# Kernel tuning notes

Measured on AMD Instinct MI355X. Metric: run time of the kernel, lower is better.

## Reference

```python
import jax, jax.numpy as jnp
import numpy as np

B, IN, H = 64, 1024, 1024

def setup_inputs() -> dict:
    key = jax.random.key(0)
    ks = jax.random.split(key, 16)
    s = 0.02
    inp = {
        'x': jax.random.normal(ks[0], (B, IN), dtype=jnp.float32),
        'C': jax.random.normal(ks[1], (B, H, H), dtype=jnp.float32) * 0.1,
        'n': jax.random.normal(ks[2], (B, H), dtype=jnp.float32) * 0.1,
        'm': jnp.zeros((B, H), dtype=jnp.float32),
    }
    names = ['i', 'f', 'o', 'q', 'k', 'v']
    for j, nm in enumerate(names):
        inp['W_' + nm] = jax.random.normal(ks[3 + 2 * j], (H, IN), dtype=jnp.float32) * s
        inp['b_' + nm] = jax.random.normal(ks[4 + 2 * j], (H,), dtype=jnp.float32) * s
    return inp

def reference(x, C, n, m, W_i, b_i, W_f, b_f, W_o, b_o, W_q, b_q, W_k, b_k, W_v, b_v):
    lin = lambda W, b: x @ W.T + b  # (B, H)
    i_tilda = lin(W_i, b_i)
    f_tilda = lin(W_f, b_f)
    o_tilda = lin(W_o, b_o)
    q_t = lin(W_q, b_q)
    k_t = lin(W_k, b_k) / jnp.sqrt(jnp.asarray(H, dtype=x.dtype))
    v_t = lin(W_v, b_v)

    f_t = jax.nn.sigmoid(f_tilda)
    o_t = jax.nn.sigmoid(o_tilda)
    # m_t = max(log(f_t) + m, log(exp(i_tilda))) = max(log_sigmoid(f_tilda) + m, i_tilda)
    m_t = jnp.maximum(jnp.log(f_t) + m, i_tilda)
    i_prime = jnp.exp(i_tilda - m_t)

    # Outer-product fast-weight update: C_t[b,i,k] = f*C + i' * v[b,i] k[b,k]
    C_t = f_t[:, :, None] * C + i_prime[:, :, None] * jnp.einsum('bi,bk->bik', v_t, k_t)
    n_t = f_t * n + i_prime * k_t

    # diagonal(n_t @ q_t.T) == per-row dot product
    normalize_inner = jnp.sum(n_t * q_t, axis=-1)
    divisor = jnp.maximum(jnp.abs(normalize_inner), jnp.ones_like(normalize_inner))
    h_tilda = jnp.einsum('bkj,bj->bk', C_t, q_t) / divisor[:, None]
    h_t = o_t * h_tilda
    return (h_t, C_t, n_t, m_t)
```

## Files before the change

### kernel.cpp

```cpp
#include <hip/hip_runtime.h>
#include <math.h>

#define BB 64
#define HH 1024
#define KK 1024

#define OFF_H ((size_t)0)
#define OFF_C ((size_t)BB * HH)
#define OFF_N (OFF_C + (size_t)BB * HH * HH)
#define OFF_M (OFF_N + (size_t)BB * HH)

#define SPLITK 4
#define GBN 32
#define GBK 64
#define NCOLBLK (6 * HH / GBN)

typedef float __attribute__((ext_vector_type(4))) f32x4;

__device__ __forceinline__ float dot4v(f32x4 a, f32x4 b) {
    return a[0] * b[0] + a[1] * b[1] + a[2] * b[2] + a[3] * b[3];
}
__device__ __forceinline__ void fma4(float4& a, const float4 x, const float4 w) {
    a.x = fmaf(x.x, w.x, a.x);
    a.y = fmaf(x.y, w.y, a.y);
    a.z = fmaf(x.z, w.z, a.z);
    a.w = fmaf(x.w, w.w, a.w);
}
__device__ __forceinline__ f32x4 ntload4(const float* p) {
    return __builtin_nontemporal_load((const f32x4*)p);
}
__device__ __forceinline__ f32x4 ld4(const float* p) {
    return *(const f32x4*)p;
}
__device__ __forceinline__ void ntstore4(float* p, f32x4 v) {
    __builtin_nontemporal_store(v, (f32x4*)p);
}

__global__ __launch_bounds__(256) void k_gemm(
    const float* __restrict__ x,
    const float* __restrict__ Wi, const float* __restrict__ Wf,
    const float* __restrict__ Wo, const float* __restrict__ Wq,
    const float* __restrict__ Wk, const float* __restrict__ Wv,
    float* __restrict__ Gp)
{
    const int cb = blockIdx.x % NCOLBLK;
    const int kc = blockIdx.x / NCOLBLK;
    const int n0 = cb * GBN;
    const int g  = n0 >> 10;
    const int h0 = n0 & (HH - 1);
    const int k0 = kc * (KK / SPLITK);

    const float* W = (g == 0) ? Wi : (g == 1) ? Wf : (g == 2) ? Wo
                   : (g == 3) ? Wq : (g == 4) ? Wk : Wv;

    const int tid = threadIdx.x;
    const int tn  = tid & 15;
    const int tm  = tid >> 4;

    __shared__ float sW[GBN][GBK + 4];

    float4 acc[4][2];
#pragma unroll
    for (int i = 0; i < 4; ++i)
#pragma unroll
        for (int j = 0; j < 2; ++j) acc[i][j] = make_float4(0.f, 0.f, 0.f, 0.f);

    for (int kk = k0; kk < k0 + KK / SPLITK; kk += GBK) {
#pragma unroll
        for (int i = 0; i < 2; ++i) {
            const int idx = tid + i * 256;
            const int c = idx >> 4;
            const int s = idx & 15;
            const f32x4 v = ntload4(W + (size_t)(h0 + c) * KK + kk + s * 4);
            *(f32x4*)&sW[c][s * 4] = v;
        }
        __syncthreads();

        const float4* xr0 = (const float4*)(x + (size_t)(tm * 4 + 0) * KK + kk);
        const float4* xr1 = (const float4*)(x + (size_t)(tm * 4 + 1) * KK + kk);
        const float4* xr2 = (const float4*)(x + (size_t)(tm * 4 + 2) * KK + kk);
        const float4* xr3 = (const float4*)(x + (size_t)(tm * 4 + 3) * KK + kk);
#pragma unroll
        for (int s = 0; s < GBK / 4; ++s) {
            const float4 w0 = *(const float4*)&sW[tn * 2 + 0][s * 4];
            const float4 w1 = *(const float4*)&sW[tn * 2 + 1][s * 4];
            const float4 a0 = xr0[s];
            const float4 a1 = xr1[s];
            const float4 a2 = xr2[s];
            const float4 a3 = xr3[s];
            fma4(acc[0][0], a0, w0); fma4(acc[0][1], a0, w1);
            fma4(acc[1][0], a1, w0); fma4(acc[1][1], a1, w1);
            fma4(acc[2][0], a2, w0); fma4(acc[2][1], a2, w1);
            fma4(acc[3][0], a3, w0); fma4(acc[3][1], a3, w1);
        }
        __syncthreads();
    }

#pragma unroll
    for (int i = 0; i < 4; ++i) {
        const int b = tm * 4 + i;
        const int h = h0 + tn * 2;
        float2 v;
        v.x = acc[i][0].x + acc[i][0].y + acc[i][0].z + acc[i][0].w;
        v.y = acc[i][1].x + acc[i][1].y + acc[i][1].z + acc[i][1].w;
        *(float2*)(Gp + ((size_t)(kc * 6 + g) * BB + b) * HH + h) = v;
    }
}

__global__ __launch_bounds__(256) void k_epilogue(
    const float* __restrict__ Gp,
    const float* __restrict__ n_in, const float* __restrict__ m_in,
    const float* __restrict__ bi, const float* __restrict__ bf,
    const float* __restrict__ bo, const float* __restrict__ bq,
    const float* __restrict__ bk, const float* __restrict__ bv,
    float* __restrict__ out,
    float* __restrict__ f_s, float* __restrict__ iv_s, float* __restrict__ o_s,
    float* __restrict__ k_s, float* __restrict__ q_s, float* __restrict__ ni4)
{
    const int b = blockIdx.x >> 2;
    const int h = ((blockIdx.x & 3) << 8) + threadIdx.x;
    const size_t bh = (size_t)b * HH + h;

    float gsum[6];
#pragma unroll
    for (int gg = 0; gg < 6; ++gg) {
        float s = 0.f;
#pragma unroll
        for (int kc = 0; kc < SPLITK; ++kc)
            s += Gp[((size_t)(kc * 6 + gg) * BB + b) * HH + h];
        gsum[gg] = s;
    }

    const float it = gsum[0] + bi[h];
    const float ft = gsum[1] + bf[h];
    const float ot = gsum[2] + bo[h];
    const float qt = gsum[3] + bq[h];
    const float kt = (gsum[4] + bk[h]) * 0.03125f;
    const float vt = gsum[5] + bv[h];

    const float fsig = 1.0f / (1.0f + expf(-ft));
    const float lsf  = (ft >= 0.0f) ? -log1pf(expf(-ft)) : (ft - log1pf(expf(ft)));
    const float mt   = fmaxf(lsf + m_in[bh], it);
    const float ip   = expf(it - mt);
    const float nt   = fsig * n_in[bh] + ip * kt;
    const float osg  = 1.0f / (1.0f + expf(-ot));

    out[OFF_N + bh] = nt;
    out[OFF_M + bh] = mt;
    f_s[bh]  = fsig;
    iv_s[bh] = ip * vt;
    o_s[bh]  = osg;
    k_s[bh]  = kt;
    q_s[bh]  = qt;

    float d = nt * qt;
#pragma unroll
    for (int off = 32; off >= 1; off >>= 1) d += __shfl_xor(d, off, 64);
    __shared__ float sd[4];
    if ((threadIdx.x & 63) == 0) sd[threadIdx.x >> 6] = d;
    __syncthreads();
    if (threadIdx.x == 0)
        ni4[blockIdx.x] = sd[0] + sd[1] + sd[2] + sd[3];
}

__global__ __launch_bounds__(256, 8) void k2_fastweight(
    const float* __restrict__ C,
    const float* __restrict__ f_s, const float* __restrict__ iv_s,
    const float* __restrict__ o_s, const float* __restrict__ k_s,
    const float* __restrict__ q_s, const float* __restrict__ ni4,
    float* __restrict__ out)
{
    const int b    = blockIdx.y;
    const int wave = threadIdx.x >> 6;
    const int lane = threadIdx.x & 63;
    const size_t row = (size_t)b * HH + blockIdx.x * 4 + wave;

    const float* Crow = C + row * HH;
    const int col = lane * 4;

    f32x4 a[4], t[4];
#pragma unroll
    for (int s = 0; s < 4; ++s) a[s] = ntload4(Crow + col + s * 256);
    const float* kr = k_s + (size_t)b * HH;
#pragma unroll
    for (int s = 0; s < 4; ++s) t[s] = ld4(kr + col + s * 256);

    const float f  = f_s[row];
    const float iv = iv_s[row];

    float* Ct = out + OFF_C + row * HH;
#pragma unroll
    for (int s = 0; s < 4; ++s) {
        a[s][0] = fmaf(f, a[s][0], iv * t[s][0]);
        a[s][1] = fmaf(f, a[s][1], iv * t[s][1]);
        a[s][2] = fmaf(f, a[s][2], iv * t[s][2]);
        a[s][3] = fmaf(f, a[s][3], iv * t[s][3]);
        ntstore4(Ct + col + s * 256, a[s]);
    }

    const float* qr = q_s + (size_t)b * HH;
#pragma unroll
    for (int s = 0; s < 4; ++s) t[s] = ld4(qr + col + s * 256);
    float d = 0.f;
#pragma unroll
    for (int s = 0; s < 4; ++s) d += dot4v(a[s], t[s]);
#pragma unroll
    for (int off = 32; off >= 1; off >>= 1) d += __shfl_xor(d, off, 64);

    if (lane == 0) {
        const float nn = fabsf(ni4[b * 4] + ni4[b * 4 + 1] +
                               ni4[b * 4 + 2] + ni4[b * 4 + 3]);
        out[OFF_H + row] = o_s[row] * d / fmaxf(nn, 1.0f);
    }
}

extern "C" void kernel_launch(void* const* d_in, const int* in_sizes, int n_in,
                              void* d_out, int out_size, void* d_ws, size_t ws_size,
                              hipStream_t stream) {
    const float* x  = (const float*)d_in[0];
    const float* C  = (const float*)d_in[1];
    const float* n  = (const float*)d_in[2];
    const float* m  = (const float*)d_in[3];
    const float* Wi = (const float*)d_in[4];  const float* bi = (const float*)d_in[5];
    const float* Wf = (const float*)d_in[6];  const float* bf = (const float*)d_in[7];
    const float* Wo = (const float*)d_in[8];  const float* bo = (const float*)d_in[9];
    const float* Wq = (const float*)d_in[10]; const float* bq = (const float*)d_in[11];
    const float* Wk = (const float*)d_in[12]; const float* bk = (const float*)d_in[13];
    const float* Wv = (const float*)d_in[14]; const float* bv = (const float*)d_in[15];

    float* out = (float*)d_out;
    float* ws  = (float*)d_ws;
    float* f_s  = ws;
    float* iv_s = ws + (size_t)BB * HH;
    float* o_s  = ws + (size_t)2 * BB * HH;
    float* k_s  = ws + (size_t)3 * BB * HH;
    float* q_s  = ws + (size_t)4 * BB * HH;
    float* ni4  = ws + (size_t)5 * BB * HH;
    float* Gp   = ws + (size_t)5 * BB * HH + 256;

    k_gemm<<<NCOLBLK * SPLITK, 256, 0, stream>>>(x, Wi, Wf, Wo, Wq, Wk, Wv, Gp);

    k_epilogue<<<BB * 4, 256, 0, stream>>>(Gp, n, m, bi, bf, bo, bq, bk, bv,
                                           out, f_s, iv_s, o_s, k_s, q_s, ni4);

    k2_fastweight<<<dim3(HH / 4, BB), 256, 0, stream>>>(C, f_s, iv_s, o_s,
                                                        k_s, q_s, ni4, out);
}
```

Measured before the change: 495.9 us.

## Map one C row per block in fast-weight kernel, use plain stores

The fast-weight kernel now launches one 256-thread block per C row, so each thread handles a single float4 instead of four, and the row dot product is reduced through shared memory and a barrier. The C_t output now uses regular stores instead of nontemporal stores. This exposes more blocks and fewer loads per thread for the bandwidth-bound C stream. In exchange it adds block-level synchronization, quadruples the block count, and may let C_t writes pollute the cache.

```diff
diff --git a/kernel.cpp b/kernel.cpp
--- a/kernel.cpp
+++ b/kernel.cpp
@@ -31,9 +31,6 @@
 }
 __device__ __forceinline__ f32x4 ld4(const float* p) {
     return *(const f32x4*)p;
-}
-__device__ __forceinline__ void ntstore4(float* p, f32x4 v) {
-    __builtin_nontemporal_store(v, (f32x4*)p);
 }
 
 __global__ __launch_bounds__(256) void k_gemm(
@@ -170,47 +167,36 @@
     const float* __restrict__ q_s, const float* __restrict__ ni4,
     float* __restrict__ out)
 {
-    const int b    = blockIdx.y;
-    const int wave = threadIdx.x >> 6;
-    const int lane = threadIdx.x & 63;
-    const size_t row = (size_t)b * HH + blockIdx.x * 4 + wave;
-
-    const float* Crow = C + row * HH;
-    const int col = lane * 4;
-
-    f32x4 a[4], t[4];
-#pragma unroll
-    for (int s = 0; s < 4; ++s) a[s] = ntload4(Crow + col + s * 256);
-    const float* kr = k_s + (size_t)b * HH;
-#pragma unroll
-    for (int s = 0; s < 4; ++s) t[s] = ld4(kr + col + s * 256);
+    const int row = blockIdx.x;
+    const int b   = row >> 10;
+    const int t   = threadIdx.x;
 
     const float f  = f_s[row];
     const float iv = iv_s[row];
 
-    float* Ct = out + OFF_C + row * HH;
-#pragma unroll
-    for (int s = 0; s < 4; ++s) {
-        a[s][0] = fmaf(f, a[s][0], iv * t[s][0]);
-        a[s][1] = fmaf(f, a[s][1], iv * t[s][1]);
-        a[s][2] = fmaf(f, a[s][2], iv * t[s][2]);
-        a[s][3] = fmaf(f, a[s][3], iv * t[s][3]);
-        ntstore4(Ct + col + s * 256, a[s]);
-    }
-
-    const float* qr = q_s + (size_t)b * HH;
-#pragma unroll
-    for (int s = 0; s < 4; ++s) t[s] = ld4(qr + col + s * 256);
-    float d = 0.f;
-#pragma unroll
-    for (int s = 0; s < 4; ++s) d += dot4v(a[s], t[s]);
+    const f32x4 c4 = ntload4(C + (size_t)row * HH + t * 4);
+    const f32x4 k4 = ld4(k_s + (size_t)b * HH + t * 4);
+    const f32x4 q4 = ld4(q_s + (size_t)b * HH + t * 4);
+
+    f32x4 o;
+    o[0] = fmaf(f, c4[0], iv * k4[0]);
+    o[1] = fmaf(f, c4[1], iv * k4[1]);
+    o[2] = fmaf(f, c4[2], iv * k4[2]);
+    o[3] = fmaf(f, c4[3], iv * k4[3]);
+    *(f32x4*)(out + OFF_C + (size_t)row * HH + t * 4) = o;
+
+    float d = dot4v(o, q4);
 #pragma unroll
     for (int off = 32; off >= 1; off >>= 1) d += __shfl_xor(d, off, 64);
 
-    if (lane == 0) {
-        const float nn = fabsf(ni4[b * 4] + ni4[b * 4 + 1] +
-                               ni4[b * 4 + 2] + ni4[b * 4 + 3]);
-        out[OFF_H + row] = o_s[row] * d / fmaxf(nn, 1.0f);
+    __shared__ float sd[4];
+    if ((t & 63) == 0) sd[t >> 6] = d;
+    __syncthreads();
+    if (t == 0) {
+        const float tot = sd[0] + sd[1] + sd[2] + sd[3];
+        const float nn  = fabsf(ni4[b * 4] + ni4[b * 4 + 1] +
+                                ni4[b * 4 + 2] + ni4[b * 4 + 3]);
+        out[OFF_H + row] = o_s[row] * tot / fmaxf(nn, 1.0f);
     }
 }
 
@@ -243,6 +229,5 @@
     k_epilogue<<<BB * 4, 256, 0, stream>>>(Gp, n, m, bi, bf, bo, bq, bk, bv,
                                            out, f_s, iv_s, o_s, k_s, q_s, ni4);
 
-    k2_fastweight<<<dim3(HH / 4, BB), 256, 0, stream>>>(C, f_s, iv_s, o_s,
-                                                        k_s, q_s, ni4, out);
-}
+    k2_fastweight<<<BB * HH, 256, 0, stream>>>(C, f_s, iv_s, o_s, k_s, q_s, ni4, out);
+}
```

Result: no change. 493.4 us (-0.5%).
